# Performance work log

Measured on AMD Instinct MI355X. Metric: run time of the kernel, lower is better.

The kernel has to match this reference:

```python
import jax, jax.numpy as jnp
import numpy as np

B, S, D_MODEL, N_HEADS, D_FF = 4, 2048, 1024, 16, 4096
HEAD_DIM = D_MODEL // N_HEADS
NUM_BUCKETS, MAX_DISTANCE = 32, 128
EPS = 1e-6


def _relative_position_bucket(relative_position, num_buckets=NUM_BUCKETS, max_distance=MAX_DISTANCE):
    # bidirectional (encoder) variant, matching T5RelativePositionBias
    n = -relative_position
    nb = num_buckets // 2
    ret = (n < 0).astype(jnp.int32) * nb
    n = jnp.abs(n)
    max_exact = nb // 2
    val_if_large = max_exact + (
        jnp.log(jnp.maximum(n, 1).astype(jnp.float32) / max_exact)
        / np.log(max_distance / max_exact) * (nb - max_exact)
    ).astype(jnp.int32)
    val_if_large = jnp.minimum(val_if_large, nb - 1)
    return ret + jnp.where(n < max_exact, n, val_if_large)


def t5_position_bias(rel_emb, q_len, k_len):
    ctx = jnp.arange(q_len)[:, None]
    mem = jnp.arange(k_len)[None, :]
    rp_bucket = _relative_position_bucket(mem - ctx)          # [S, S]
    bias = rel_emb[rp_bucket]                                  # [S, S, H]
    return jnp.transpose(bias, (2, 0, 1))[None]                # [1, H, S, S]


def layer_norm(x, g, b):
    mu = jnp.mean(x, axis=-1, keepdims=True)
    var = jnp.mean(jnp.square(x - mu), axis=-1, keepdims=True)
    return (x - mu) * jax.lax.rsqrt(var + EPS) * g + b


def setup_inputs() -> dict:
    key = jax.random.key(0)
    ks = jax.random.split(key, 20)
    s = 0.02
    p = {
        'src': jax.random.normal(ks[0], (B, S, D_MODEL), jnp.float32),
        'wq': jax.random.normal(ks[1], (D_MODEL, D_MODEL), jnp.float32) * s,
        'bq': jnp.zeros((D_MODEL,), jnp.float32),
        'wk': jax.random.normal(ks[2], (D_MODEL, D_MODEL), jnp.float32) * s,
        'bk': jnp.zeros((D_MODEL,), jnp.float32),
        'wv': jax.random.normal(ks[3], (D_MODEL, D_MODEL), jnp.float32) * s,
        'bv': jnp.zeros((D_MODEL,), jnp.float32),
        'wo': jax.random.normal(ks[4], (D_MODEL, D_MODEL), jnp.float32) * s,
        'bo': jnp.zeros((D_MODEL,), jnp.float32),
        'w1': jax.random.normal(ks[5], (D_MODEL, D_FF), jnp.float32) * s,
        'b1': jnp.zeros((D_FF,), jnp.float32),
        'w2': jax.random.normal(ks[6], (D_FF, D_MODEL), jnp.float32) * s,
        'b2': jnp.zeros((D_MODEL,), jnp.float32),
        'ln1_g': jnp.ones((D_MODEL,), jnp.float32),
        'ln1_b': jnp.zeros((D_MODEL,), jnp.float32),
        'ln2_g': jnp.ones((D_MODEL,), jnp.float32),
        'ln2_b': jnp.zeros((D_MODEL,), jnp.float32),
        'rel_emb': jax.random.normal(ks[7], (NUM_BUCKETS, N_HEADS), jnp.float32) * s,
    }
    return p


def reference(src, wq, bq, wk, bk, wv, bv, wo, bo, w1, b1, w2, b2,
              ln1_g, ln1_b, ln2_g, ln2_b, rel_emb):
    b, s, _ = src.shape

    # --- self-attention block (pre-norm) ---
    xn = layer_norm(src, ln1_g, ln1_b)
    q = (xn @ wq + bq).reshape(b, s, N_HEADS, HEAD_DIM).transpose(0, 2, 1, 3)
    k = (xn @ wk + bk).reshape(b, s, N_HEADS, HEAD_DIM).transpose(0, 2, 1, 3)
    v = (xn @ wv + bv).reshape(b, s, N_HEADS, HEAD_DIM).transpose(0, 2, 1, 3)

    bias = t5_position_bias(rel_emb, s, s)                       # [1,H,S,S]
    scores = jnp.einsum('bhqd,bhkd->bhqk', q, k) / np.sqrt(HEAD_DIM) + bias
    attn = jax.nn.softmax(scores, axis=-1)
    ctx = jnp.einsum('bhqk,bhkd->bhqd', attn, v)                 # [B,H,S,Dh]
    ctx = ctx.transpose(0, 2, 1, 3).reshape(b, s, D_MODEL)
    x = src + (ctx @ wo + bo)

    # --- FFN block (pre-norm, ReLU) ---
    yn = layer_norm(x, ln2_g, ln2_b)
    y = jax.nn.relu(yn @ w1 + b1) @ w2 + b2
    return x + y
```

## Files before the change

kernel.cpp:

```cpp
#include <hip/hip_runtime.h>
#include <math.h>

typedef unsigned short u16;

#define S_LEN 2048
#define BSZ 4
#define DM 1024
#define NH 16
#define HD 64
#define DFF 4096
#define ROWS (BSZ * S_LEN)
#define LOG2E 1.4426950408889634f

typedef __attribute__((__ext_vector_type__(8))) __bf16 bf16x8;
typedef __attribute__((__ext_vector_type__(8))) short short8;
typedef __attribute__((__ext_vector_type__(4))) short short4v;
typedef __attribute__((__ext_vector_type__(4))) float f32x4;
typedef __attribute__((__ext_vector_type__(4))) float float4v;

__device__ __forceinline__ float bf2f(u16 u) {
    union { unsigned int i; float f; } c; c.i = ((unsigned int)u) << 16; return c.f;
}
__device__ __forceinline__ u16 f2bf(float f) {
    union { float f; unsigned int i; } c; c.f = f;
    unsigned int r = c.i + 0x7fffu + ((c.i >> 16) & 1u);
    return (u16)(r >> 16);
}
__device__ __forceinline__ u16 f2bf_cvt(float f) {
    __bf16 h = (__bf16)f;
    return __builtin_bit_cast(u16, h);
}
__device__ __forceinline__ float ldin(const void* p, long i, int f32) {
    return f32 ? ((const float*)p)[i] : bf2f(((const u16*)p)[i]);
}
__device__ __forceinline__ int dtype_f32(const u16* ln1g) {
    return ln1g[0] != 0x3F80;
}
__device__ __forceinline__ void gl_lds16(const void* g, void* l) {
    __builtin_amdgcn_global_load_lds(
        (const __attribute__((address_space(1))) unsigned int*)g,
        (__attribute__((address_space(3))) unsigned int*)l, 16, 0, 0);
}

#define BARR  asm volatile("s_barrier" ::: "memory")
#define LGKM0 asm volatile("s_waitcnt lgkmcnt(0)" ::: "memory")
#define VM4   asm volatile("s_waitcnt vmcnt(4)" ::: "memory")
#define VM2   asm volatile("s_waitcnt vmcnt(2)" ::: "memory")
#define VM0   asm volatile("s_waitcnt vmcnt(0)" ::: "memory")

__device__ __forceinline__ void tr_tile(
    const void* __restrict__ src, u16* __restrict__ dst, int N, int K,
    int bx, int by, int f32, int tid, u16 (*t)[72])
{
#pragma unroll
    for (int i = 0; i < 2; i++) {
        int c = tid + i * 256;
        int row = c >> 3, col = (c & 7) * 8;
        long off = (long)(by * 64 + row) * N + bx * 64 + col;
        short8 v;
        if (f32) {
            const float* s = (const float*)src + off;
            float4v a = *(const float4v*)s;
            float4v b = *(const float4v*)(s + 4);
#pragma unroll
            for (int k = 0; k < 4; k++) { v[k] = (short)f2bf(a[k]); v[k + 4] = (short)f2bf(b[k]); }
        } else {
            v = *(const short8*)((const u16*)src + off);
        }
        *(short8*)(&t[row][col]) = v;
    }
    __syncthreads();
#pragma unroll
    for (int i = 0; i < 2; i++) {
        int c = tid + i * 256;
        int row = c >> 3, col = (c & 7) * 8;
        short8 v;
#pragma unroll
        for (int jj = 0; jj < 8; jj++) v[jj] = (short)t[col + jj][row];
        *(short8*)(dst + (long)(bx * 64 + row) * K + by * 64 + col) = v;
    }
}

__global__ __launch_bounds__(256) void transpose4(
    const void* wq, const void* wk, const void* wv, const void* wo,
    u16* __restrict__ wqkvt, u16* __restrict__ wot, const u16* __restrict__ ln1g)
{
    __shared__ u16 t[64][72];
    int z = blockIdx.z;
    const void* src = (z == 0) ? wq : (z == 1) ? wk : (z == 2) ? wv : wo;
    u16* dst = (z < 3) ? wqkvt + (long)z * 1024 * 1024 : wot;
    tr_tile(src, dst, DM, DM, blockIdx.x, blockIdx.y, dtype_f32(ln1g), threadIdx.x, t);
}

__global__ __launch_bounds__(256) void transpose2(
    const void* w1, const void* w2, u16* __restrict__ w1t, u16* __restrict__ w2t,
    const u16* __restrict__ ln1g)
{
    __shared__ u16 t[64][72];
    int f32 = dtype_f32(ln1g);
    if (blockIdx.z == 0)
        tr_tile(w1, w1t, DFF, DM, blockIdx.x, blockIdx.y, f32, threadIdx.x, t);
    else
        tr_tile(w2, w2t, DM, DFF, blockIdx.y, blockIdx.x, f32, threadIdx.x, t);
}

__global__ __launch_bounds__(256) void vtrans(
    const u16* __restrict__ v, u16* __restrict__ vt)
{
    __shared__ u16 t[64][72];
    int s0 = blockIdx.x * 64;
    int bh = blockIdx.y;
    const u16* src = v + (long)bh * S_LEN * HD;
    u16* dst = vt + (long)bh * HD * S_LEN;
    int tid = threadIdx.x;
#pragma unroll
    for (int i = 0; i < 2; i++) {
        int c = tid + i * 256;
        int row = c >> 3, col = (c & 7) * 8;
        *(short8*)(&t[row][col]) = *(const short8*)(src + (long)(s0 + row) * HD + col);
    }
    __syncthreads();
#pragma unroll
    for (int i = 0; i < 2; i++) {
        int c = tid + i * 256;
        int row = c >> 3, col = (c & 7) * 8;
        short8 o;
#pragma unroll
        for (int jj = 0; jj < 8; jj++) o[jj] = (short)t[col + jj][row];
        *(short8*)(dst + (long)row * S_LEN + s0 + col) = o;
    }
}

__global__ __launch_bounds__(256) void prep_kernel(
    const void* bq, const void* bk, const void* bv, const void* bo,
    const void* b1, const void* b2, const void* l1g, const void* l1b,
    const void* l2g, const void* l2b, const void* rel,
    u16* __restrict__ smalls, float* __restrict__ bias_full)
{
    int f32 = dtype_f32((const u16*)l1g);
    int tid = blockIdx.x * blockDim.x + threadIdx.x;
    if (tid < 13312) {
        float v;
        if      (tid < 1024)  v = ldin(bq,  tid,         f32);
        else if (tid < 2048)  v = ldin(bk,  tid - 1024,  f32);
        else if (tid < 3072)  v = ldin(bv,  tid - 2048,  f32);
        else if (tid < 4096)  v = ldin(bo,  tid - 3072,  f32);
        else if (tid < 8192)  v = ldin(b1,  tid - 4096,  f32);
        else if (tid < 9216)  v = ldin(b2,  tid - 8192,  f32);
        else if (tid < 10240) v = ldin(l1g, tid - 9216,  f32);
        else if (tid < 11264) v = ldin(l1b, tid - 10240, f32);
        else if (tid < 12288) v = ldin(l2g, tid - 11264, f32);
        else                  v = ldin(l2b, tid - 12288, f32);
        smalls[tid] = f2bf(v);
    }
    if (tid < 4095 * 16) {
        int dIdx = tid >> 4;
        int h = tid & 15;
        int delta = dIdx - 2047;
        int n = -delta;
        int ret = (n < 0) ? 16 : 0;
        int na = (n < 0) ? -n : n;
        int bkt;
        if (na < 8) {
            bkt = na;
        } else {
            float tval = logf((float)na * 0.125f) * 2.8853900817779268f;
            int v = 8 + (int)tval;
            bkt = v < 15 ? v : 15;
        }
        bkt += ret;
        bias_full[h * 4095 + dIdx] = ldin(rel, bkt * 16 + h, f32) * LOG2E;
    }
}

__global__ __launch_bounds__(256) void ln_kernel(
    const void* __restrict__ xin, int external, const u16* __restrict__ ln1g,
    const u16* __restrict__ g, const u16* __restrict__ bta, u16* __restrict__ out)
{
    int f32 = external ? dtype_f32(ln1g) : 0;
    int row = blockIdx.x;
    int tid = threadIdx.x;
    float vals[4];
    if (f32) {
        float4v v = *(const float4v*)((const float*)xin + (long)row * DM + tid * 4);
#pragma unroll
        for (int k = 0; k < 4; k++) vals[k] = v[k];
    } else {
        short4v v = *(const short4v*)((const u16*)xin + (long)row * DM + tid * 4);
#pragma unroll
        for (int k = 0; k < 4; k++) vals[k] = bf2f((u16)v[k]);
    }
    float s1 = 0.f, s2 = 0.f;
#pragma unroll
    for (int k = 0; k < 4; k++) { s1 += vals[k]; s2 += vals[k] * vals[k]; }
#pragma unroll
    for (int off = 32; off > 0; off >>= 1) {
        s1 += __shfl_xor(s1, off);
        s2 += __shfl_xor(s2, off);
    }
    __shared__ float ps1[4], ps2[4];
    int wave = tid >> 6, lane = tid & 63;
    if (lane == 0) { ps1[wave] = s1; ps2[wave] = s2; }
    __syncthreads();
    s1 = ps1[0] + ps1[1] + ps1[2] + ps1[3];
    s2 = ps2[0] + ps2[1] + ps2[2] + ps2[3];
    float mu = s1 * (1.0f / DM);
    float var = s2 * (1.0f / DM) - mu * mu;
    float rs = rsqrtf(var + 1e-6f);
    short4v ov;
#pragma unroll
    for (int k = 0; k < 4; k++) {
        float gv = bf2f(g[tid * 4 + k]);
        float bv = bf2f(bta[tid * 4 + k]);
        ov[k] = (short)f2bf((vals[k] - mu) * rs * gv + bv);
    }
    *(short4v*)(out + (long)row * DM + tid * 4) = ov;
}

#define TM 256
#define TN 256
#define TK 64

#define PHASE(bi, q, STAGE, WAITV)                                             \
    {                                                                          \
        if ((q) == 0) {                                                        \
            _Pragma("unroll")                                                  \
            for (int j = 0; j < 4; j++) {                                      \
                _Pragma("unroll")                                              \
                for (int t = 0; t < 2; t++)                                    \
                    bfr[j][t] = __builtin_bit_cast(bf16x8, *(const short8*)(   \
                        &Bs[bi][wn * 64 + j * 16 + l16][((t * 4 + quad) ^ rxor) * 8])); \
            }                                                                  \
        }                                                                      \
        _Pragma("unroll")                                                      \
        for (int i = 0; i < 2; i++) {                                          \
            _Pragma("unroll")                                                  \
            for (int t = 0; t < 2; t++)                                        \
                af[i][t] = __builtin_bit_cast(bf16x8, *(const short8*)(        \
                    &As[bi][wm * 128 + ((q) * 2 + i) * 16 + l16][((t * 4 + quad) ^ rxor) * 8])); \
        }                                                                      \
        STAGE                                                                  \
        WAITV;                                                                 \
        BARR;                                                                  \
        LGKM0;                                                                 \
        __builtin_amdgcn_sched_barrier(0);                                     \
        __builtin_amdgcn_s_setprio(1);                                         \
        _Pragma("unroll")                                                      \
        for (int i = 0; i < 2; i++) {                                          \
            _Pragma("unroll")                                                  \
            for (int j = 0; j < 4; j++) {                                      \
                acc[(q) * 2 + i][j] = __builtin_amdgcn_mfma_f32_16x16x32_bf16( \
                    af[i][0], bfr[j][0], acc[(q) * 2 + i][j], 0, 0, 0);        \
                acc[(q) * 2 + i][j] = __builtin_amdgcn_mfma_f32_16x16x32_bf16( \
                    af[i][1], bfr[j][1], acc[(q) * 2 + i][j], 0, 0, 0);        \
            }                                                                  \
        }                                                                      \
        __builtin_amdgcn_s_setprio(0);                                         \
        BARR;                                                                  \
    }

__global__ __launch_bounds__(512, 2) void gemm256(
    const u16* __restrict__ A, const u16* __restrict__ Bt,
    const u16* __restrict__ bias, int M, int N, int K, int mode,
    u16* __restrict__ out_q, u16* __restrict__ out_k, u16* __restrict__ out_v,
    u16* __restrict__ outp)
{
    __shared__ u16 As[2][TM][TK];
    __shared__ u16 Bs[2][TN][TK];

    int tid = threadIdx.x;
    int wavei = tid >> 6, lane = tid & 63;
    int quad = lane >> 4, l16 = lane & 15;
    int wm = wavei >> 2, wn = wavei & 3;

    int nwg = gridDim.x * gridDim.y;
    int bid = blockIdx.y * gridDim.x + blockIdx.x;
    int chunk = nwg >> 3;
    int swz = (bid & 7) * chunk + (bid >> 3);
    int bx = swz % gridDim.x, by = swz / gridDim.x;
    long m0 = (long)by * TM, n0 = (long)bx * TN;

    int srow = tid >> 3;
    int pchk = tid & 7;
    int cchk = pchk ^ (srow & 7);
    int rxor = l16 & 7;

    int NT = K / TK;

    auto stageA = [&](int bufi, int h, int t) {
        const u16* g = A + (m0 + h * 128 + srow) * (long)K + (long)t * TK + cchk * 8;
        gl_lds16(g,                 &As[bufi][h * 128 + srow     ][pchk * 8]);
        gl_lds16(g + 64 * (long)K,  &As[bufi][h * 128 + srow + 64][pchk * 8]);
    };
    auto stageB = [&](int bufi, int h, int t) {
        const u16* g = Bt + (n0 + h * 128 + srow) * (long)K + (long)t * TK + cchk * 8;
        gl_lds16(g,                 &Bs[bufi][h * 128 + srow     ][pchk * 8]);
        gl_lds16(g + 64 * (long)K,  &Bs[bufi][h * 128 + srow + 64][pchk * 8]);
    };

    f32x4 acc[8][4];
    f32x4 z = {0.f, 0.f, 0.f, 0.f};
#pragma unroll
    for (int i = 0; i < 8; i++)
#pragma unroll
        for (int j = 0; j < 4; j++) acc[i][j] = z;

    bf16x8 bfr[4][2];
    bf16x8 af[2][2];

    stageA(0, 0, 0); stageA(0, 1, 0); stageB(0, 0, 0); stageB(0, 1, 0);
    stageB(1, 0, 1); stageB(1, 1, 1);
    VM4;
    BARR;

    for (int kt = 0; kt < NT - 2; kt += 2) {
        PHASE(0, 0, { stageA(1, 0, kt + 1); stageA(1, 1, kt + 1); }, (void)0);
        PHASE(0, 1, { stageB(0, 0, kt + 2); }, (void)0);
        PHASE(0, 2, { stageB(0, 1, kt + 2); }, (void)0);
        PHASE(0, 3, {}, VM4);
        PHASE(1, 0, { stageA(0, 0, kt + 2); }, (void)0);
        PHASE(1, 1, { stageA(0, 1, kt + 2); stageB(1, 0, kt + 3); }, (void)0);
        PHASE(1, 2, { stageB(1, 1, kt + 3); }, (void)0);
        PHASE(1, 3, {}, VM4);
    }
    PHASE(0, 0, { stageA(1, 0, NT - 1); stageA(1, 1, NT - 1); }, (void)0);
    PHASE(0, 1, {}, (void)0);
    PHASE(0, 2, {}, (void)0);
    PHASE(0, 3, {}, VM0);
    PHASE(1, 0, {}, (void)0);
    PHASE(1, 1, {}, (void)0);
    PHASE(1, 2, {}, (void)0);
    PHASE(1, 3, {}, (void)0);

#pragma unroll
    for (int i = 0; i < 8; i++) {
#pragma unroll
        for (int j = 0; j < 4; j++) {
#pragma unroll
            for (int r = 0; r < 4; r++) {
                long gr = m0 + wm * 128 + i * 16 + quad * 4 + r;
                long gc = n0 + wn * 64 + j * 16 + l16;
                float val = acc[i][j][r] + bf2f(bias[gc]);
                if (mode == 1) {
                    int sel = (int)(gc >> 10);
                    int cc = (int)(gc & 1023);
                    int h = cc >> 6, d = cc & 63;
                    int b = (int)(gr >> 11), s = (int)(gr & 2047);
                    u16* dst = (sel == 0) ? out_q : (sel == 1 ? out_k : out_v);
                    dst[(((long)(b * NH + h)) * S_LEN + s) * HD + d] = f2bf(val);
                } else {
                    outp[gr * (long)N + gc] = f2bf(val > 0.f ? val : 0.f);
                }
            }
        }
    }
}

#define NBM 256
#define NBN 128

#define PHN(bi, half, STAGE, WAITV)                                            \
    {                                                                          \
        if ((half) == 0) {                                                     \
            _Pragma("unroll")                                                  \
            for (int j = 0; j < 2; j++) {                                      \
                _Pragma("unroll")                                              \
                for (int t = 0; t < 2; t++)                                    \
                    nbfr[j][t] = __builtin_bit_cast(bf16x8, *(const short8*)(  \
                        &Bs[bi][wn * 32 + j * 16 + l16][((t * 4 + quad) ^ rxor) * 8])); \
            }                                                                  \
        }                                                                      \
        _Pragma("unroll")                                                      \
        for (int i = 0; i < 4; i++) {                                          \
            _Pragma("unroll")                                                  \
            for (int t = 0; t < 2; t++)                                        \
                naf[i][t] = __builtin_bit_cast(bf16x8, *(const short8*)(       \
                    &As[bi][wm * 128 + ((half) * 4 + i) * 16 + l16][((t * 4 + quad) ^ rxor) * 8])); \
        }                                                                      \
        STAGE                                                                  \
        WAITV;                                                                 \
        BARR;                                                                  \
        LGKM0;                                                                 \
        __builtin_amdgcn_sched_barrier(0);                                     \
        __builtin_amdgcn_s_setprio(1);                                         \
        _Pragma("unroll")                                                      \
        for (int i = 0; i < 4; i++) {                                          \
            _Pragma("unroll")                                                  \
            for (int j = 0; j < 2; j++) {                                      \
                acc[(half) * 4 + i][j] = __builtin_amdgcn_mfma_f32_16x16x32_bf16( \
                    naf[i][0], nbfr[j][0], acc[(half) * 4 + i][j], 0, 0, 0);   \
                acc[(half) * 4 + i][j] = __builtin_amdgcn_mfma_f32_16x16x32_bf16( \
                    naf[i][1], nbfr[j][1], acc[(half) * 4 + i][j], 0, 0, 0);   \
            }                                                                  \
        }                                                                      \
        __builtin_amdgcn_s_setprio(0);                                         \
        BARR;                                                                  \
    }

__global__ __launch_bounds__(512, 2) void gemm256n(
    const u16* __restrict__ A, const u16* __restrict__ Bt,
    const u16* __restrict__ bias, int M, int N, int K, int mode,
    const void* __restrict__ res, void* __restrict__ outp,
    const u16* __restrict__ ln1g)
{
    __shared__ u16 As[2][NBM][TK];
    __shared__ u16 Bs[2][NBN][TK];

    int tid = threadIdx.x;
    int wavei = tid >> 6, lane = tid & 63;
    int quad = lane >> 4, l16 = lane & 15;
    int wm = wavei >> 2, wn = wavei & 3;

    int nwg = gridDim.x * gridDim.y;
    int bid = blockIdx.y * gridDim.x + blockIdx.x;
    int chunk = nwg >> 3;
    int swz = (bid & 7) * chunk + (bid >> 3);
    int bx = swz % gridDim.x, by = swz / gridDim.x;
    long m0 = (long)by * NBM, n0 = (long)bx * NBN;
    int flg = dtype_f32(ln1g);

    int srow = tid >> 3;
    int pchk = tid & 7;
    int cchk = pchk ^ (srow & 7);
    int rxor = l16 & 7;

    int NT = K / TK;

    auto stageA = [&](int bufi, int h, int t) {
        const u16* g = A + (m0 + h * 128 + srow) * (long)K + (long)t * TK + cchk * 8;
        gl_lds16(g,                 &As[bufi][h * 128 + srow     ][pchk * 8]);
        gl_lds16(g + 64 * (long)K,  &As[bufi][h * 128 + srow + 64][pchk * 8]);
    };
    auto stageB = [&](int bufi, int t) {
        const u16* g = Bt + (n0 + srow) * (long)K + (long)t * TK + cchk * 8;
        gl_lds16(g,                 &Bs[bufi][srow     ][pchk * 8]);
        gl_lds16(g + 64 * (long)K,  &Bs[bufi][srow + 64][pchk * 8]);
    };

    f32x4 acc[8][2];
    f32x4 z = {0.f, 0.f, 0.f, 0.f};
#pragma unroll
    for (int i = 0; i < 8; i++)
#pragma unroll
        for (int j = 0; j < 2; j++) acc[i][j] = z;

    bf16x8 nbfr[2][2];
    bf16x8 naf[4][2];

    stageA(0, 0, 0); stageA(0, 1, 0); stageB(0, 0);
    stageB(1, 1);
    VM2;
    BARR;

    for (int kt = 0; kt < NT - 2; kt += 2) {
        PHN(0, 0, { stageA(1, 0, kt + 1); stageA(1, 1, kt + 1); }, (void)0);
        PHN(0, 1, { stageB(0, kt + 2); }, VM2);
        PHN(1, 0, { stageA(0, 0, kt + 2); stageA(0, 1, kt + 2); }, (void)0);
        PHN(1, 1, { stageB(1, kt + 3); }, VM2);
    }
    PHN(0, 0, { stageA(1, 0, NT - 1); stageA(1, 1, NT - 1); }, (void)0);
    PHN(0, 1, {}, VM0);
    PHN(1, 0, {}, (void)0);
    PHN(1, 1, {}, (void)0);

#pragma unroll
    for (int i = 0; i < 8; i++) {
#pragma unroll
        for (int j = 0; j < 2; j++) {
#pragma unroll
            for (int r = 0; r < 4; r++) {
                long gr = m0 + wm * 128 + i * 16 + quad * 4 + r;
                long gc = n0 + wn * 32 + j * 16 + l16;
                float val = acc[i][j][r] + bf2f(bias[gc]);
                long idx = gr * (long)N + gc;
                if (mode == 2) {
                    float rv = flg ? ((const float*)res)[idx]
                                   : bf2f(((const u16*)res)[idx]);
                    ((u16*)outp)[idx] = f2bf(val + rv);
                } else {
                    float o = val + bf2f(((const u16*)res)[idx]);
                    if (flg) ((float*)outp)[idx] = o;
                    else     ((u16*)outp)[idx]  = f2bf(o);
                }
            }
        }
    }
}

__global__ __launch_bounds__(256, 4) void attn_kernel(
    const u16* __restrict__ Qg, const u16* __restrict__ Kg, const u16* __restrict__ Vtg,
    const float* __restrict__ bias_full, u16* __restrict__ ctx)
{
    __shared__ u16 Ks[64][64];
    __shared__ u16 Vt[64][64];
    __shared__ u16 Ps[64][72];
    __shared__ u16 bias_s[2112];

    int bh = blockIdx.y;
    int b = bh >> 4, h = bh & 15;
    int q0 = blockIdx.x * 64;
    const u16* Q  = Qg  + (long)bh * S_LEN * HD;
    const u16* Kp = Kg  + (long)bh * S_LEN * HD;
    const u16* Vp = Vtg + (long)bh * HD * S_LEN;

    int tid = threadIdx.x;
    int wave = tid >> 6, lane = tid & 63;
    int quad = lane >> 4, l16 = lane & 15;

    for (int i = tid; i < 2112; i += 256)
        bias_s[i] = f2bf(bias_full[h * 4095 + 1984 + i - q0]);
    float Bneg = bias_full[h * 4095 + 0];
    float Bpos = bias_full[h * 4095 + 4094];

    int prow = tid >> 3, pchk = tid & 7;
    int cchk = pchk ^ (prow & 7);
    int rxor = l16 & 7;
    int rc0 = (quad ^ rxor) * 8;
    int rc1 = ((4 + quad) ^ rxor) * 8;

    bf16x8 aq[2];
#pragma unroll
    for (int t = 0; t < 2; t++)
        aq[t] = __builtin_bit_cast(bf16x8,
            *(const short8*)(Q + (long)(q0 + wave * 16 + l16) * HD + t * 32 + quad * 8));

    bf16x8 ones;
#pragma unroll
    for (int i = 0; i < 8; i++) ones[i] = (__bf16)1.0f;

    f32x4 o[4];
    f32x4 z = {0.f, 0.f, 0.f, 0.f};
#pragma unroll
    for (int j = 0; j < 4; j++) o[j] = z;
    f32x4 lacc = z;

    int ib = 63 + quad * 4 - wave * 16 - l16;
    const float c0 = 0.125f * LOG2E;

    auto compute = [&](int t0) {
        f32x4 s_[4];
#pragma unroll
        for (int j = 0; j < 4; j++) {
            f32x4 a = z;
            bf16x8 kf0 = __builtin_bit_cast(bf16x8, *(const short8*)(&Ks[j * 16 + l16][rc0]));
            a = __builtin_amdgcn_mfma_f32_16x16x32_bf16(kf0, aq[0], a, 0, 0, 0);
            bf16x8 kf1 = __builtin_bit_cast(bf16x8, *(const short8*)(&Ks[j * 16 + l16][rc1]));
            a = __builtin_amdgcn_mfma_f32_16x16x32_bf16(kf1, aq[1], a, 0, 0, 0);
            s_[j] = a;
        }
        int d0 = t0 - q0;
        int nearb = (d0 >= -153 && d0 <= 153);
        float bconst = (d0 > 0) ? Bpos : Bneg;
#pragma unroll
        for (int j = 0; j < 4; j++) {
            short4v pk;
#pragma unroll
            for (int r = 0; r < 4; r++) {
                float bl = nearb ? bf2f(bias_s[ib + t0 + j * 16 + r]) : bconst;
                float p = __builtin_amdgcn_exp2f(fmaf(s_[j][r], c0, bl));
                pk[r] = (short)f2bf_cvt(p);
            }
            *(short4v*)(&Ps[wave * 16 + l16][j * 16 + quad * 4]) = pk;
        }
        bf16x8 ap[2];
#pragma unroll
        for (int tt = 0; tt < 2; tt++)
            ap[tt] = __builtin_bit_cast(bf16x8,
                *(const short8*)(&Ps[wave * 16 + l16][tt * 32 + quad * 8]));
        lacc = __builtin_amdgcn_mfma_f32_16x16x32_bf16(ap[0], ones, lacc, 0, 0, 0);
        lacc = __builtin_amdgcn_mfma_f32_16x16x32_bf16(ap[1], ones, lacc, 0, 0, 0);
#pragma unroll
        for (int j = 0; j < 4; j++) {
            f32x4 t = o[j];
            bf16x8 bv0 = __builtin_bit_cast(bf16x8, *(const short8*)(&Vt[j * 16 + l16][rc0]));
            t = __builtin_amdgcn_mfma_f32_16x16x32_bf16(ap[0], bv0, t, 0, 0, 0);
            bf16x8 bv1 = __builtin_bit_cast(bf16x8, *(const short8*)(&Vt[j * 16 + l16][rc1]));
            t = __builtin_amdgcn_mfma_f32_16x16x32_bf16(ap[1], bv1, t, 0, 0, 0);
            o[j] = t;
        }
    };

    short8 ka0, ka1, va0, va1, kb0, kb1, vb0, vb1;
    ka0 = *(const short8*)(Kp + (long)(prow) * HD + cchk * 8);
    ka1 = *(const short8*)(Kp + (long)(32 + prow) * HD + cchk * 8);
    va0 = *(const short8*)(Vp + (long)(prow) * S_LEN + cchk * 8);
    va1 = *(const short8*)(Vp + (long)(32 + prow) * S_LEN + cchk * 8);

    for (int t0 = 0; t0 < S_LEN; t0 += 128) {
        if (t0 > 0) BARR;
        VM0;
        *(short8*)(&Ks[prow][pchk * 8])      = ka0;
        *(short8*)(&Ks[32 + prow][pchk * 8]) = ka1;
        *(short8*)(&Vt[prow][pchk * 8])      = va0;
        *(short8*)(&Vt[32 + prow][pchk * 8]) = va1;
        {
            int t1 = t0 + 64;
            kb0 = *(const short8*)(Kp + (long)(t1 + prow) * HD + cchk * 8);
            kb1 = *(const short8*)(Kp + (long)(t1 + 32 + prow) * HD + cchk * 8);
            vb0 = *(const short8*)(Vp + (long)(prow) * S_LEN + t1 + cchk * 8);
            vb1 = *(const short8*)(Vp + (long)(32 + prow) * S_LEN + t1 + cchk * 8);
        }
        LGKM0; BARR;
        compute(t0);

        BARR;
        VM0;
        *(short8*)(&Ks[prow][pchk * 8])      = kb0;
        *(short8*)(&Ks[32 + prow][pchk * 8]) = kb1;
        *(short8*)(&Vt[prow][pchk * 8])      = vb0;
        *(short8*)(&Vt[32 + prow][pchk * 8]) = vb1;
        if (t0 + 128 < S_LEN) {
            int t2 = t0 + 128;
            ka0 = *(const short8*)(Kp + (long)(t2 + prow) * HD + cchk * 8);
            ka1 = *(const short8*)(Kp + (long)(t2 + 32 + prow) * HD + cchk * 8);
            va0 = *(const short8*)(Vp + (long)(prow) * S_LEN + t2 + cchk * 8);
            va1 = *(const short8*)(Vp + (long)(32 + prow) * S_LEN + t2 + cchk * 8);
        }
        LGKM0; BARR;
        compute(t0 + 64);
    }

#pragma unroll
    for (int r = 0; r < 4; r++) {
        int qr = wave * 16 + quad * 4 + r;
        float linv = 1.0f / lacc[r];
        long srow2 = (long)(b * S_LEN + q0 + qr);
#pragma unroll
        for (int j = 0; j < 4; j++)
            ctx[srow2 * DM + h * HD + j * 16 + l16] = f2bf(o[j][r] * linv);
    }
}

extern "C" void kernel_launch(void* const* d_in, const int* in_sizes, int n_in,
                              void* d_out, int out_size, void* d_ws, size_t ws_size,
                              hipStream_t stream)
{
    const void* src  = d_in[0];
    const void* wq   = d_in[1];
    const void* bq   = d_in[2];
    const void* wk   = d_in[3];
    const void* bk   = d_in[4];
    const void* wv   = d_in[5];
    const void* bv   = d_in[6];
    const void* wo   = d_in[7];
    const void* bo   = d_in[8];
    const void* w1   = d_in[9];
    const void* b1   = d_in[10];
    const void* w2   = d_in[11];
    const void* b2   = d_in[12];
    const void* ln1g = d_in[13];
    const void* ln1b = d_in[14];
    const void* ln2g = d_in[15];
    const void* ln2b = d_in[16];
    const void* rel  = d_in[17];
    const u16* l1g16 = (const u16*)ln1g;

    char* ws = (char*)d_ws;
    const long MB = 1L << 20;
    u16*   smalls = (u16*)  (ws);
    float* bfull  = (float*)(ws + 65536);
    u16*   xn     = (u16*)  (ws + 1  * MB);
    u16*   vtg    = (u16*)  (ws + 1  * MB);
    u16*   qws    = (u16*)  (ws + 17 * MB);
    u16*   kws    = (u16*)  (ws + 33 * MB);
    u16*   vws    = (u16*)  (ws + 49 * MB);
    u16*   hbuf   = (u16*)  (ws + 1  * MB);
    u16*   ctx    = (u16*)  (ws + 65 * MB);
    u16*   yn     = (u16*)  (ws + 65 * MB);
    u16*   xbf    = (u16*)  (ws + 81 * MB);
    u16*   wqkvt  = (u16*)  (ws + 97 * MB);
    u16*   wot    = (u16*)  (ws + 103 * MB);
    u16*   w1t    = (u16*)  (ws + 97 * MB);
    u16*   w2t    = (u16*)  (ws + 105 * MB);

    transpose4<<<dim3(16, 16, 4), 256, 0, stream>>>(wq, wk, wv, wo, wqkvt, wot, l1g16);
    prep_kernel<<<256, 256, 0, stream>>>(bq, bk, bv, bo, b1, b2,
                                         ln1g, ln1b, ln2g, ln2b, rel,
                                         smalls, bfull);

    ln_kernel<<<ROWS, 256, 0, stream>>>(src, 1, l1g16,
                                        smalls + 9216, smalls + 10240, xn);

    gemm256<<<dim3(3072 / TN, ROWS / TM), 512, 0, stream>>>(
        xn, wqkvt, smalls + 0, ROWS, 3072, DM, 1, qws, kws, vws, nullptr);

    vtrans<<<dim3(S_LEN / 64, BSZ * NH), 256, 0, stream>>>(vws, vtg);

    attn_kernel<<<dim3(S_LEN / 64, BSZ * NH), 256, 0, stream>>>(qws, kws, vtg, bfull, ctx);

    gemm256n<<<dim3(DM / NBN, ROWS / NBM), 512, 0, stream>>>(
        ctx, wot, smalls + 3072, ROWS, DM, DM, 2, src, xbf, l1g16);

    transpose2<<<dim3(64, 16, 2), 256, 0, stream>>>(w1, w2, w1t, w2t, l1g16);

    ln_kernel<<<ROWS, 256, 0, stream>>>(xbf, 0, l1g16,
                                        smalls + 11264, smalls + 12288, yn);

    gemm256<<<dim3(DFF / TN, ROWS / TM), 512, 0, stream>>>(
        yn, w1t, smalls + 4096, ROWS, DFF, DM, 3, nullptr, nullptr, nullptr, hbuf);

    gemm256n<<<dim3(DM / NBN, ROWS / NBM), 512, 0, stream>>>(
        hbuf, w2t, smalls + 8192, ROWS, DM, DFF, 4, xbf, d_out, l1g16);
}
```

Measured before the change: 583.1 us.

## Double attention query tile to 128 and run QKV projection through gemm256n

The attention kernel now runs 512 threads (8 waves) per block over 128 query rows. Each K/V tile in LDS is shared by twice as many queries, and loading is split so half the threads load K and half load V. The bias window and near-band bounds are widened to match. The QKV projection also moves to the gemm256n kernel with a new mode that scatters Q/K/V into head-major layout. Larger blocks and more LDS (Ps doubles) may reduce occupancy, and the scattered epilogue stores are strided.

```diff
diff --git a/kernel.cpp b/kernel.cpp
--- a/kernel.cpp
+++ b/kernel.cpp
@@ -400,6 +400,7 @@
 __global__ __launch_bounds__(512, 2) void gemm256n(
     const u16* __restrict__ A, const u16* __restrict__ Bt,
     const u16* __restrict__ bias, int M, int N, int K, int mode,
+    u16* __restrict__ out_q, u16* __restrict__ out_k, u16* __restrict__ out_v,
     const void* __restrict__ res, void* __restrict__ outp,
     const u16* __restrict__ ln1g)
 {
@@ -417,7 +418,7 @@
     int swz = (bid & 7) * chunk + (bid >> 3);
     int bx = swz % gridDim.x, by = swz / gridDim.x;
     long m0 = (long)by * NBM, n0 = (long)bx * NBN;
-    int flg = dtype_f32(ln1g);
+    int flg = (mode == 2 || mode == 4) ? dtype_f32(ln1g) : 0;
 
     int srow = tid >> 3;
     int pchk = tid & 7;
@@ -472,12 +473,20 @@
                 long gr = m0 + wm * 128 + i * 16 + quad * 4 + r;
                 long gc = n0 + wn * 32 + j * 16 + l16;
                 float val = acc[i][j][r] + bf2f(bias[gc]);
-                long idx = gr * (long)N + gc;
-                if (mode == 2) {
+                if (mode == 1) {
+                    int sel = (int)(gc >> 10);
+                    int cc = (int)(gc & 1023);
+                    int h = cc >> 6, d = cc & 63;
+                    int b = (int)(gr >> 11), s = (int)(gr & 2047);
+                    u16* dst = (sel == 0) ? out_q : (sel == 1 ? out_k : out_v);
+                    dst[(((long)(b * NH + h)) * S_LEN + s) * HD + d] = f2bf(val);
+                } else if (mode == 2) {
+                    long idx = gr * (long)N + gc;
                     float rv = flg ? ((const float*)res)[idx]
                                    : bf2f(((const u16*)res)[idx]);
                     ((u16*)outp)[idx] = f2bf(val + rv);
                 } else {
+                    long idx = gr * (long)N + gc;
                     float o = val + bf2f(((const u16*)res)[idx]);
                     if (flg) ((float*)outp)[idx] = o;
                     else     ((u16*)outp)[idx]  = f2bf(o);
@@ -487,18 +496,18 @@
     }
 }
 
-__global__ __launch_bounds__(256, 4) void attn_kernel(
+__global__ __launch_bounds__(512, 8) void attn_kernel(
     const u16* __restrict__ Qg, const u16* __restrict__ Kg, const u16* __restrict__ Vtg,
     const float* __restrict__ bias_full, u16* __restrict__ ctx)
 {
     __shared__ u16 Ks[64][64];
     __shared__ u16 Vt[64][64];
-    __shared__ u16 Ps[64][72];
-    __shared__ u16 bias_s[2112];
+    __shared__ u16 Ps[128][72];
+    __shared__ u16 bias_s[2176];
 
     int bh = blockIdx.y;
     int b = bh >> 4, h = bh & 15;
-    int q0 = blockIdx.x * 64;
+    int q0 = blockIdx.x * 128;
     const u16* Q  = Qg  + (long)bh * S_LEN * HD;
     const u16* Kp = Kg  + (long)bh * S_LEN * HD;
     const u16* Vp = Vtg + (long)bh * HD * S_LEN;
@@ -507,12 +516,14 @@
     int wave = tid >> 6, lane = tid & 63;
     int quad = lane >> 4, l16 = lane & 15;
 
-    for (int i = tid; i < 2112; i += 256)
-        bias_s[i] = f2bf(bias_full[h * 4095 + 1984 + i - q0]);
+    for (int i = tid; i < 2176; i += 512)
+        bias_s[i] = f2bf(bias_full[h * 4095 + 1920 + i - q0]);
     float Bneg = bias_full[h * 4095 + 0];
     float Bpos = bias_full[h * 4095 + 4094];
 
-    int prow = tid >> 3, pchk = tid & 7;
+    int isv = wave >= 4;
+    int t2 = tid & 255;
+    int prow = t2 >> 3, pchk = t2 & 7;
     int cchk = pchk ^ (prow & 7);
     int rxor = l16 & 7;
     int rc0 = (quad ^ rxor) * 8;
@@ -534,7 +545,7 @@
     for (int j = 0; j < 4; j++) o[j] = z;
     f32x4 lacc = z;
 
-    int ib = 63 + quad * 4 - wave * 16 - l16;
+    int ib = 127 + quad * 4 - wave * 16 - l16;
     const float c0 = 0.125f * LOG2E;
 
     auto compute = [&](int t0) {
@@ -549,7 +560,7 @@
             s_[j] = a;
         }
         int d0 = t0 - q0;
-        int nearb = (d0 >= -153 && d0 <= 153);
+        int nearb = (d0 >= -153 && d0 <= 217);
         float bconst = (d0 > 0) ? Bpos : Bneg;
 #pragma unroll
         for (int j = 0; j < 4; j++) {
@@ -580,41 +591,37 @@
         }
     };
 
-    short8 ka0, ka1, va0, va1, kb0, kb1, vb0, vb1;
-    ka0 = *(const short8*)(Kp + (long)(prow) * HD + cchk * 8);
-    ka1 = *(const short8*)(Kp + (long)(32 + prow) * HD + cchk * 8);
-    va0 = *(const short8*)(Vp + (long)(prow) * S_LEN + cchk * 8);
-    va1 = *(const short8*)(Vp + (long)(32 + prow) * S_LEN + cchk * 8);
+    auto ld0 = [&](int t) -> short8 {
+        return isv ? *(const short8*)(Vp + (long)prow * S_LEN + t + cchk * 8)
+                   : *(const short8*)(Kp + (long)(t + prow) * HD + cchk * 8);
+    };
+    auto ld1 = [&](int t) -> short8 {
+        return isv ? *(const short8*)(Vp + (long)(32 + prow) * S_LEN + t + cchk * 8)
+                   : *(const short8*)(Kp + (long)(t + 32 + prow) * HD + cchk * 8);
+    };
+    u16* dst0 = isv ? &Vt[prow][pchk * 8] : &Ks[prow][pchk * 8];
+    u16* dst1 = isv ? &Vt[32 + prow][pchk * 8] : &Ks[32 + prow][pchk * 8];
+
+    short8 sa0 = ld0(0), sa1 = ld1(0);
+    short8 sb0, sb1;
 
     for (int t0 = 0; t0 < S_LEN; t0 += 128) {
         if (t0 > 0) BARR;
         VM0;
-        *(short8*)(&Ks[prow][pchk * 8])      = ka0;
-        *(short8*)(&Ks[32 + prow][pchk * 8]) = ka1;
-        *(short8*)(&Vt[prow][pchk * 8])      = va0;
-        *(short8*)(&Vt[32 + prow][pchk * 8]) = va1;
-        {
-            int t1 = t0 + 64;
-            kb0 = *(const short8*)(Kp + (long)(t1 + prow) * HD + cchk * 8);
-            kb1 = *(const short8*)(Kp + (long)(t1 + 32 + prow) * HD + cchk * 8);
-            vb0 = *(const short8*)(Vp + (long)(prow) * S_LEN + t1 + cchk * 8);
-            vb1 = *(const short8*)(Vp + (long)(32 + prow) * S_LEN + t1 + cchk * 8);
-        }
+        *(short8*)dst0 = sa0;
+        *(short8*)dst1 = sa1;
+        sb0 = ld0(t0 + 64);
+        sb1 = ld1(t0 + 64);
         LGKM0; BARR;
         compute(t0);
 
         BARR;
         VM0;
-        *(short8*)(&Ks[prow][pchk * 8])      = kb0;
-        *(short8*)(&Ks[32 + prow][pchk * 8]) = kb1;
-        *(short8*)(&Vt[prow][pchk * 8])      = vb0;
-        *(short8*)(&Vt[32 + prow][pchk * 8]) = vb1;
+        *(short8*)dst0 = sb0;
+        *(short8*)dst1 = sb1;
         if (t0 + 128 < S_LEN) {
-            int t2 = t0 + 128;
-            ka0 = *(const short8*)(Kp + (long)(t2 + prow) * HD + cchk * 8);
-            ka1 = *(const short8*)(Kp + (long)(t2 + 32 + prow) * HD + cchk * 8);
-            va0 = *(const short8*)(Vp + (long)(prow) * S_LEN + t2 + cchk * 8);
-            va1 = *(const short8*)(Vp + (long)(32 + prow) * S_LEN + t2 + cchk * 8);
+            sa0 = ld0(t0 + 128);
+            sa1 = ld1(t0 + 128);
         }
         LGKM0; BARR;
         compute(t0 + 64);
@@ -681,15 +688,17 @@
     ln_kernel<<<ROWS, 256, 0, stream>>>(src, 1, l1g16,
                                         smalls + 9216, smalls + 10240, xn);
 
-    gemm256<<<dim3(3072 / TN, ROWS / TM), 512, 0, stream>>>(
-        xn, wqkvt, smalls + 0, ROWS, 3072, DM, 1, qws, kws, vws, nullptr);
+    gemm256n<<<dim3(3072 / NBN, ROWS / NBM), 512, 0, stream>>>(
+        xn, wqkvt, smalls + 0, ROWS, 3072, DM, 1,
+        qws, kws, vws, nullptr, nullptr, l1g16);
 
     vtrans<<<dim3(S_LEN / 64, BSZ * NH), 256, 0, stream>>>(vws, vtg);
 
-    attn_kernel<<<dim3(S_LEN / 64, BSZ * NH), 256, 0, stream>>>(qws, kws, vtg, bfull, ctx);
+    attn_kernel<<<dim3(S_LEN / 128, BSZ * NH), 512, 0, stream>>>(qws, kws, vtg, bfull, ctx);
 
     gemm256n<<<dim3(DM / NBN, ROWS / NBM), 512, 0, stream>>>(
-        ctx, wot, smalls + 3072, ROWS, DM, DM, 2, src, xbf, l1g16);
+        ctx, wot, smalls + 3072, ROWS, DM, DM, 2,
+        nullptr, nullptr, nullptr, src, xbf, l1g16);
 
     transpose2<<<dim3(64, 16, 2), 256, 0, stream>>>(w1, w2, w1t, w2t, l1g16);
 
@@ -700,5 +709,6 @@
         yn, w1t, smalls + 4096, ROWS, DFF, DM, 3, nullptr, nullptr, nullptr, hbuf);
 
     gemm256n<<<dim3(DM / NBN, ROWS / NBM), 512, 0, stream>>>(
-        hbuf, w2t, smalls + 8192, ROWS, DM, DFF, 4, xbf, d_out, l1g16);
-}
+        hbuf, w2t, smalls + 8192, ROWS, DM, DFF, 4,
+        nullptr, nullptr, nullptr, xbf, d_out, l1g16);
+}
```

Result: slower. 769.0 us (+31.9%).
